# Kernel tuning notes

Measured on AMD Instinct MI355X. Metric: run time of the kernel, lower is better.

The kernel has to match this reference:

```python
import jax, jax.numpy as jnp
import numpy as np

N = 8192        # nodes
F_IN = 128      # input features (layers_dims[0])
F_OUT = 64      # per-head output features (layers_dims[1])
H = 4           # nheads
ALPHA = 0.2     # leaky relu slope
DENSITY = 0.01  # edge density for the random graph


def setup_inputs() -> dict:
    key = jax.random.key(0)
    kx, ka, kw, k1, k2 = jax.random.split(key, 5)
    x = jax.random.normal(kx, (N, F_IN), dtype=jnp.float32)
    adj = (jax.random.uniform(ka, (N, N)) < DENSITY).astype(jnp.float32)
    adj = jnp.maximum(adj, jnp.eye(N, dtype=jnp.float32))
    W = jax.random.normal(kw, (H, F_IN, F_OUT), dtype=jnp.float32) * (1.0 / np.sqrt(F_IN))
    a1 = jax.random.normal(k1, (H, F_OUT), dtype=jnp.float32) * (1.0 / np.sqrt(F_OUT))
    a2 = jax.random.normal(k2, (H, F_OUT), dtype=jnp.float32) * (1.0 / np.sqrt(F_OUT))
    return {"x": x, "adj": adj, "W": W, "a1": a1, "a2": a2}


def reference(x, adj, W, a1, a2):
    # Dropout layers are identity in eval mode (training=False).
    # Per-head projection: Wh[h] = x @ W[h]  -> [H, N, F_OUT]
    Wh = jnp.einsum('nf,hfo->hno', x, W)
    # e_ij = leakyReLU(a1 . Wh_i + a2 . Wh_j) via rank-1 broadcast (classic GAT trick)
    f1 = jnp.einsum('hno,ho->hn', Wh, a1)   # [H, N] (dst contribution)
    f2 = jnp.einsum('hno,ho->hn', Wh, a2)   # [H, N] (src contribution)
    e = f1[:, :, None] + f2[:, None, :]     # [H, N, N]
    e = jnp.where(e > 0, e, ALPHA * e)      # leaky relu
    # mask non-edges, softmax over neighbors (last axis)
    e = jnp.where(adj[None, :, :] > 0, e, jnp.float32(-1e9))
    att = jax.nn.softmax(e, axis=-1)        # [H, N, N]
    # aggregate and apply elu (concat=True branch)
    out = jnp.einsum('hnm,hmo->hno', att, Wh)  # [H, N, F_OUT]
    out = jax.nn.elu(out)
    # concat heads on feature dim -> [N, H*F_OUT]
    return jnp.transpose(out, (1, 0, 2)).reshape(N, H * F_OUT)
```

## Files before the change

### kernel.cpp

```cpp
#include <hip/hip_runtime.h>
#include <math.h>

#define N_NODES 8192
#define F_IN    128
#define F_OUT   64
#define NH      4
#define FC      256
#define MAXDEG  512

__global__ __launch_bounds__(256) void k_proj(const float* __restrict__ x,
                                              const float* __restrict__ W,
                                              float* __restrict__ Wh) {
    __shared__ float xs[16][128];
    __shared__ float ws[32][256];
    const int t = threadIdx.x;
    const int row0 = blockIdx.x * 16;

    {
        const float4* xg = (const float4*)(x + (size_t)row0 * F_IN);
        float4* xls = (float4*)&xs[0][0];
        xls[t]       = xg[t];
        xls[t + 256] = xg[t + 256];
    }

    const int tx = t & 31;
    const int ty = t >> 5;
    const int c0 = tx * 8;
    const int r0 = ty * 2;

    float acc[2][8];
#pragma unroll
    for (int r = 0; r < 2; r++)
#pragma unroll
        for (int c = 0; c < 8; c++) acc[r][c] = 0.f;

    for (int kt = 0; kt < 4; kt++) {
        __syncthreads();
        for (int q = t; q < 2048; q += 256) {
            int krow = q >> 6;
            int c4 = (q & 63) * 4;
            int h = c4 >> 6;
            int o = c4 & 63;
            float4 v = *(const float4*)(W + (size_t)h * (F_IN * F_OUT)
                                          + (size_t)(kt * 32 + krow) * F_OUT + o);
            *(float4*)&ws[krow][c4] = v;
        }
        __syncthreads();
#pragma unroll
        for (int kk4 = 0; kk4 < 8; kk4++) {
            float4 xa0 = *(const float4*)&xs[r0][kt * 32 + kk4 * 4];
            float4 xa1 = *(const float4*)&xs[r0 + 1][kt * 32 + kk4 * 4];
            float a0k[4] = {xa0.x, xa0.y, xa0.z, xa0.w};
            float a1k[4] = {xa1.x, xa1.y, xa1.z, xa1.w};
#pragma unroll
            for (int kkk = 0; kkk < 4; kkk++) {
                int wrow = kk4 * 4 + kkk;
                float4 b0 = *(const float4*)&ws[wrow][c0];
                float4 b1 = *(const float4*)&ws[wrow][c0 + 4];
                float a0 = a0k[kkk], a1v = a1k[kkk];
                acc[0][0] += a0 * b0.x; acc[0][1] += a0 * b0.y;
                acc[0][2] += a0 * b0.z; acc[0][3] += a0 * b0.w;
                acc[0][4] += a0 * b1.x; acc[0][5] += a0 * b1.y;
                acc[0][6] += a0 * b1.z; acc[0][7] += a0 * b1.w;
                acc[1][0] += a1v * b0.x; acc[1][1] += a1v * b0.y;
                acc[1][2] += a1v * b0.z; acc[1][3] += a1v * b0.w;
                acc[1][4] += a1v * b1.x; acc[1][5] += a1v * b1.y;
                acc[1][6] += a1v * b1.z; acc[1][7] += a1v * b1.w;
            }
        }
    }

#pragma unroll
    for (int r = 0; r < 2; r++) {
        float4 v0 = make_float4(acc[r][0], acc[r][1], acc[r][2], acc[r][3]);
        float4 v1 = make_float4(acc[r][4], acc[r][5], acc[r][6], acc[r][7]);
        size_t base = (size_t)(row0 + r0 + r) * FC + c0;
        *(float4*)&Wh[base]     = v0;
        *(float4*)&Wh[base + 4] = v1;
    }
}

__global__ __launch_bounds__(256) void k_f(const float* __restrict__ Wh,
                                           const float* __restrict__ a1,
                                           const float* __restrict__ a2,
                                           float* __restrict__ f1,
                                           float* __restrict__ f2) {
    const int wv = threadIdx.x >> 6;
    const int lane = threadIdx.x & 63;
    const int idx = blockIdx.x * 4 + wv;
    const int n = idx >> 2;
    const int h = idx & 3;
    float w = Wh[(size_t)n * FC + h * F_OUT + lane];
    float s1 = w * a1[h * F_OUT + lane];
    float s2 = w * a2[h * F_OUT + lane];
#pragma unroll
    for (int d = 32; d > 0; d >>= 1) {
        s1 += __shfl_xor(s1, d, 64);
        s2 += __shfl_xor(s2, d, 64);
    }
    if (lane == 0) {
        f1[idx] = s1;
        f2[idx] = s2;
    }
}

__global__ __launch_bounds__(256) void k_gat(const float* __restrict__ adj,
                                             const float* __restrict__ Wh,
                                             const float* __restrict__ f1,
                                             const float* __restrict__ f2,
                                             float* __restrict__ out) {
    __shared__ int cnt;
    __shared__ int jlist[MAXDEG];
    __shared__ float pbuf[NH][MAXDEG];

    const int i = blockIdx.x;
    const int t = threadIdx.x;
    if (t == 0) cnt = 0;
    __syncthreads();

    const float4* arow = (const float4*)(adj + (size_t)i * N_NODES);
    for (int q = t; q < N_NODES / 4; q += 256) {
        float4 v = arow[q];
        int jb = q * 4;
        if (v.x > 0.f) { int p = atomicAdd(&cnt, 1); if (p < MAXDEG) jlist[p] = jb; }
        if (v.y > 0.f) { int p = atomicAdd(&cnt, 1); if (p < MAXDEG) jlist[p] = jb + 1; }
        if (v.z > 0.f) { int p = atomicAdd(&cnt, 1); if (p < MAXDEG) jlist[p] = jb + 2; }
        if (v.w > 0.f) { int p = atomicAdd(&cnt, 1); if (p < MAXDEG) jlist[p] = jb + 3; }
    }
    __syncthreads();
    const int deg = min(cnt, MAXDEG);

    const int h = t >> 6;
    const int lane = t & 63;
    const float f1i = f1[i * 4 + h];

    float m = -1e30f;
    for (int e = lane; e < deg; e += 64) {
        int j = jlist[e];
        float s = f1i + f2[j * 4 + h];
        s = s > 0.f ? s : 0.2f * s;
        pbuf[h][e] = s;
        m = fmaxf(m, s);
    }
#pragma unroll
    for (int d = 32; d > 0; d >>= 1) m = fmaxf(m, __shfl_xor(m, d, 64));

    float l = 0.f;
    for (int e = lane; e < deg; e += 64) {
        float pv = __expf(pbuf[h][e] - m);
        pbuf[h][e] = pv;
        l += pv;
    }
#pragma unroll
    for (int d = 32; d > 0; d >>= 1) l += __shfl_xor(l, d, 64);
    const float inv = 1.f / l;

    __syncthreads();

    float acc0 = 0.f, acc1 = 0.f, acc2 = 0.f, acc3 = 0.f;
    const float* whh = Wh + h * F_OUT + lane;
    int e = 0;
    for (; e + 4 <= deg; e += 4) {
        int j0 = jlist[e], j1 = jlist[e + 1], j2 = jlist[e + 2], j3 = jlist[e + 3];
        float p0 = pbuf[h][e], p1 = pbuf[h][e + 1], p2 = pbuf[h][e + 2], p3 = pbuf[h][e + 3];
        float w0 = whh[(size_t)j0 * FC];
        float w1 = whh[(size_t)j1 * FC];
        float w2 = whh[(size_t)j2 * FC];
        float w3 = whh[(size_t)j3 * FC];
        acc0 += p0 * w0; acc1 += p1 * w1; acc2 += p2 * w2; acc3 += p3 * w3;
    }
    for (; e < deg; e++) {
        acc0 += pbuf[h][e] * whh[(size_t)jlist[e] * FC];
    }
    float v = (acc0 + acc1 + acc2 + acc3) * inv;
    v = v > 0.f ? v : (expf(v) - 1.f);
    out[(size_t)i * FC + t] = v;
}

extern "C" void kernel_launch(void* const* d_in, const int* in_sizes, int n_in,
                              void* d_out, int out_size, void* d_ws, size_t ws_size,
                              hipStream_t stream) {
    const float* x   = (const float*)d_in[0];
    const float* adj = (const float*)d_in[1];
    const float* W   = (const float*)d_in[2];
    const float* a1  = (const float*)d_in[3];
    const float* a2  = (const float*)d_in[4];
    float* out = (float*)d_out;

    float* Wh = (float*)d_ws;
    float* f1 = Wh + (size_t)N_NODES * FC;
    float* f2 = f1 + (size_t)N_NODES * NH;

    k_proj<<<N_NODES / 16, 256, 0, stream>>>(x, W, Wh);
    k_f<<<N_NODES, 256, 0, stream>>>(Wh, a1, a2, f1, f2);
    k_gat<<<N_NODES, 256, 0, stream>>>(adj, Wh, f1, f2, out);
}
```

Baseline: 430.0 us.

## Fuse attention-score projection into GEMM and gather bf16 features in aggregation

Computes f1/f2 inside the projection kernel via a cross-lane reduction, removing the separate k_f launch. Writes a bf16 copy of Wh and gathers it in the attention kernel to halve neighbor-gather bytes. Also uses nontemporal loads for the adjacency stream, drops a redundant barrier, and uses fast exp in ELU. Trades precision of the aggregation for bandwidth and still writes an unused fp32 Wh.

```diff
diff --git a/kernel.cpp b/kernel.cpp
--- a/kernel.cpp
+++ b/kernel.cpp
@@ -1,4 +1,5 @@
 #include <hip/hip_runtime.h>
+#include <hip/hip_bf16.h>
 #include <math.h>
 
 #define N_NODES 8192
@@ -8,9 +9,16 @@
 #define FC      256
 #define MAXDEG  512
 
+typedef float f32x4 __attribute__((ext_vector_type(4)));
+
 __global__ __launch_bounds__(256) void k_proj(const float* __restrict__ x,
                                               const float* __restrict__ W,
-                                              float* __restrict__ Wh) {
+                                              const float* __restrict__ a1,
+                                              const float* __restrict__ a2,
+                                              float* __restrict__ Wh,
+                                              __hip_bfloat16* __restrict__ Wh16,
+                                              float* __restrict__ f1,
+                                              float* __restrict__ f2) {
     __shared__ float xs[16][128];
     __shared__ float ws[32][256];
     const int t = threadIdx.x;
@@ -23,89 +31,87 @@
         xls[t + 256] = xg[t + 256];
     }
 
-    const int tx = t & 31;
-    const int ty = t >> 5;
-    const int c0 = tx * 8;
-    const int r0 = ty * 2;
-
-    float acc[2][8];
-#pragma unroll
-    for (int r = 0; r < 2; r++)
-#pragma unroll
-        for (int c = 0; c < 8; c++) acc[r][c] = 0.f;
+    const int tx = t & 63;
+    const int ty = t >> 6;
+    const int c0 = tx * 4;
+    const int r0 = ty * 4;
+    const int h  = tx >> 4;
+
+    float acc[4][4];
+#pragma unroll
+    for (int r = 0; r < 4; r++)
+#pragma unroll
+        for (int c = 0; c < 4; c++) acc[r][c] = 0.f;
 
     for (int kt = 0; kt < 4; kt++) {
         __syncthreads();
         for (int q = t; q < 2048; q += 256) {
             int krow = q >> 6;
             int c4 = (q & 63) * 4;
-            int h = c4 >> 6;
-            int o = c4 & 63;
-            float4 v = *(const float4*)(W + (size_t)h * (F_IN * F_OUT)
-                                          + (size_t)(kt * 32 + krow) * F_OUT + o);
-            *(float4*)&ws[krow][c4] = v;
+            int hh = c4 >> 6;
+            int o  = c4 & 63;
+            *(float4*)&ws[krow][c4] =
+                *(const float4*)(W + (size_t)hh * (F_IN * F_OUT)
+                                   + (size_t)(kt * 32 + krow) * F_OUT + o);
         }
         __syncthreads();
 #pragma unroll
-        for (int kk4 = 0; kk4 < 8; kk4++) {
-            float4 xa0 = *(const float4*)&xs[r0][kt * 32 + kk4 * 4];
-            float4 xa1 = *(const float4*)&xs[r0 + 1][kt * 32 + kk4 * 4];
+        for (int kg = 0; kg < 8; kg++) {
+            const int kb = kt * 32 + kg * 4;
+            float4 xa0 = *(const float4*)&xs[r0 + 0][kb];
+            float4 xa1 = *(const float4*)&xs[r0 + 1][kb];
+            float4 xa2 = *(const float4*)&xs[r0 + 2][kb];
+            float4 xa3 = *(const float4*)&xs[r0 + 3][kb];
             float a0k[4] = {xa0.x, xa0.y, xa0.z, xa0.w};
             float a1k[4] = {xa1.x, xa1.y, xa1.z, xa1.w};
-#pragma unroll
-            for (int kkk = 0; kkk < 4; kkk++) {
-                int wrow = kk4 * 4 + kkk;
-                float4 b0 = *(const float4*)&ws[wrow][c0];
-                float4 b1 = *(const float4*)&ws[wrow][c0 + 4];
-                float a0 = a0k[kkk], a1v = a1k[kkk];
-                acc[0][0] += a0 * b0.x; acc[0][1] += a0 * b0.y;
-                acc[0][2] += a0 * b0.z; acc[0][3] += a0 * b0.w;
-                acc[0][4] += a0 * b1.x; acc[0][5] += a0 * b1.y;
-                acc[0][6] += a0 * b1.z; acc[0][7] += a0 * b1.w;
-                acc[1][0] += a1v * b0.x; acc[1][1] += a1v * b0.y;
-                acc[1][2] += a1v * b0.z; acc[1][3] += a1v * b0.w;
-                acc[1][4] += a1v * b1.x; acc[1][5] += a1v * b1.y;
-                acc[1][6] += a1v * b1.z; acc[1][7] += a1v * b1.w;
+            float a2k[4] = {xa2.x, xa2.y, xa2.z, xa2.w};
+            float a3k[4] = {xa3.x, xa3.y, xa3.z, xa3.w};
+#pragma unroll
+            for (int kk = 0; kk < 4; kk++) {
+                float4 b = *(const float4*)&ws[kg * 4 + kk][c0];
+                acc[0][0] += a0k[kk] * b.x; acc[0][1] += a0k[kk] * b.y;
+                acc[0][2] += a0k[kk] * b.z; acc[0][3] += a0k[kk] * b.w;
+                acc[1][0] += a1k[kk] * b.x; acc[1][1] += a1k[kk] * b.y;
+                acc[1][2] += a1k[kk] * b.z; acc[1][3] += a1k[kk] * b.w;
+                acc[2][0] += a2k[kk] * b.x; acc[2][1] += a2k[kk] * b.y;
+                acc[2][2] += a2k[kk] * b.z; acc[2][3] += a2k[kk] * b.w;
+                acc[3][0] += a3k[kk] * b.x; acc[3][1] += a3k[kk] * b.y;
+                acc[3][2] += a3k[kk] * b.z; acc[3][3] += a3k[kk] * b.w;
             }
         }
     }
 
-#pragma unroll
-    for (int r = 0; r < 2; r++) {
-        float4 v0 = make_float4(acc[r][0], acc[r][1], acc[r][2], acc[r][3]);
-        float4 v1 = make_float4(acc[r][4], acc[r][5], acc[r][6], acc[r][7]);
-        size_t base = (size_t)(row0 + r0 + r) * FC + c0;
-        *(float4*)&Wh[base]     = v0;
-        *(float4*)&Wh[base + 4] = v1;
+    float a1c[4], a2c[4];
+#pragma unroll
+    for (int c = 0; c < 4; c++) { a1c[c] = a1[c0 + c]; a2c[c] = a2[c0 + c]; }
+
+#pragma unroll
+    for (int r = 0; r < 4; r++) {
+        const int row = row0 + r0 + r;
+        float4 v = make_float4(acc[r][0], acc[r][1], acc[r][2], acc[r][3]);
+        *(float4*)&Wh[(size_t)row * FC + c0] = v;
+        union { __hip_bfloat16 hv[4]; uint2 u; } pk;
+        pk.hv[0] = __float2bfloat16(v.x); pk.hv[1] = __float2bfloat16(v.y);
+        pk.hv[2] = __float2bfloat16(v.z); pk.hv[3] = __float2bfloat16(v.w);
+        *(uint2*)(Wh16 + (size_t)row * FC + c0) = pk.u;
+        float s1 = acc[r][0] * a1c[0] + acc[r][1] * a1c[1]
+                 + acc[r][2] * a1c[2] + acc[r][3] * a1c[3];
+        float s2 = acc[r][0] * a2c[0] + acc[r][1] * a2c[1]
+                 + acc[r][2] * a2c[2] + acc[r][3] * a2c[3];
+#pragma unroll
+        for (int d = 1; d < 16; d <<= 1) {
+            s1 += __shfl_xor(s1, d, 64);
+            s2 += __shfl_xor(s2, d, 64);
+        }
+        if ((tx & 15) == 0) {
+            f1[row * NH + h] = s1;
+            f2[row * NH + h] = s2;
+        }
     }
 }
 
-__global__ __launch_bounds__(256) void k_f(const float* __restrict__ Wh,
-                                           const float* __restrict__ a1,
-                                           const float* __restrict__ a2,
-                                           float* __restrict__ f1,
-                                           float* __restrict__ f2) {
-    const int wv = threadIdx.x >> 6;
-    const int lane = threadIdx.x & 63;
-    const int idx = blockIdx.x * 4 + wv;
-    const int n = idx >> 2;
-    const int h = idx & 3;
-    float w = Wh[(size_t)n * FC + h * F_OUT + lane];
-    float s1 = w * a1[h * F_OUT + lane];
-    float s2 = w * a2[h * F_OUT + lane];
-#pragma unroll
-    for (int d = 32; d > 0; d >>= 1) {
-        s1 += __shfl_xor(s1, d, 64);
-        s2 += __shfl_xor(s2, d, 64);
-    }
-    if (lane == 0) {
-        f1[idx] = s1;
-        f2[idx] = s2;
-    }
-}
-
 __global__ __launch_bounds__(256) void k_gat(const float* __restrict__ adj,
-                                             const float* __restrict__ Wh,
+                                             const __hip_bfloat16* __restrict__ Wh16,
                                              const float* __restrict__ f1,
                                              const float* __restrict__ f2,
                                              float* __restrict__ out) {
@@ -118,9 +124,9 @@
     if (t == 0) cnt = 0;
     __syncthreads();
 
-    const float4* arow = (const float4*)(adj + (size_t)i * N_NODES);
+    const f32x4* arow = (const f32x4*)(adj + (size_t)i * N_NODES);
     for (int q = t; q < N_NODES / 4; q += 256) {
-        float4 v = arow[q];
+        f32x4 v = __builtin_nontemporal_load(&arow[q]);
         int jb = q * 4;
         if (v.x > 0.f) { int p = atomicAdd(&cnt, 1); if (p < MAXDEG) jlist[p] = jb; }
         if (v.y > 0.f) { int p = atomicAdd(&cnt, 1); if (p < MAXDEG) jlist[p] = jb + 1; }
@@ -132,12 +138,12 @@
 
     const int h = t >> 6;
     const int lane = t & 63;
-    const float f1i = f1[i * 4 + h];
+    const float f1i = f1[i * NH + h];
 
     float m = -1e30f;
     for (int e = lane; e < deg; e += 64) {
         int j = jlist[e];
-        float s = f1i + f2[j * 4 + h];
+        float s = f1i + f2[j * NH + h];
         s = s > 0.f ? s : 0.2f * s;
         pbuf[h][e] = s;
         m = fmaxf(m, s);
@@ -155,25 +161,24 @@
     for (int d = 32; d > 0; d >>= 1) l += __shfl_xor(l, d, 64);
     const float inv = 1.f / l;
 
-    __syncthreads();
-
     float acc0 = 0.f, acc1 = 0.f, acc2 = 0.f, acc3 = 0.f;
-    const float* whh = Wh + h * F_OUT + lane;
+    const __hip_bfloat16* whh = Wh16 + h * F_OUT + lane;
     int e = 0;
     for (; e + 4 <= deg; e += 4) {
         int j0 = jlist[e], j1 = jlist[e + 1], j2 = jlist[e + 2], j3 = jlist[e + 3];
-        float p0 = pbuf[h][e], p1 = pbuf[h][e + 1], p2 = pbuf[h][e + 2], p3 = pbuf[h][e + 3];
-        float w0 = whh[(size_t)j0 * FC];
-        float w1 = whh[(size_t)j1 * FC];
-        float w2 = whh[(size_t)j2 * FC];
-        float w3 = whh[(size_t)j3 * FC];
+        float p0 = pbuf[h][e], p1 = pbuf[h][e + 1];
+        float p2 = pbuf[h][e + 2], p3 = pbuf[h][e + 3];
+        float w0 = __bfloat162float(whh[(size_t)j0 * FC]);
+        float w1 = __bfloat162float(whh[(size_t)j1 * FC]);
+        float w2 = __bfloat162float(whh[(size_t)j2 * FC]);
+        float w3 = __bfloat162float(whh[(size_t)j3 * FC]);
         acc0 += p0 * w0; acc1 += p1 * w1; acc2 += p2 * w2; acc3 += p3 * w3;
     }
-    for (; e < deg; e++) {
-        acc0 += pbuf[h][e] * whh[(size_t)jlist[e] * FC];
-    }
+    for (; e < deg; e++)
+        acc0 += pbuf[h][e] * __bfloat162float(whh[(size_t)jlist[e] * FC]);
+
     float v = (acc0 + acc1 + acc2 + acc3) * inv;
-    v = v > 0.f ? v : (expf(v) - 1.f);
+    v = v > 0.f ? v : (__expf(v) - 1.f);
     out[(size_t)i * FC + t] = v;
 }
 
@@ -188,10 +193,10 @@
     float* out = (float*)d_out;
 
     float* Wh = (float*)d_ws;
-    float* f1 = Wh + (size_t)N_NODES * FC;
+    __hip_bfloat16* Wh16 = (__hip_bfloat16*)(Wh + (size_t)N_NODES * FC);
+    float* f1 = (float*)(Wh16 + (size_t)N_NODES * FC);
     float* f2 = f1 + (size_t)N_NODES * NH;
 
-    k_proj<<<N_NODES / 16, 256, 0, stream>>>(x, W, Wh);
-    k_f<<<N_NODES, 256, 0, stream>>>(Wh, a1, a2, f1, f2);
-    k_gat<<<N_NODES, 256, 0, stream>>>(adj, Wh, f1, f2, out);
+    k_proj<<<N_NODES / 16, 256, 0, stream>>>(x, W, a1, a2, Wh, Wh16, f1, f2);
+    k_gat<<<N_NODES, 256, 0, stream>>>(adj, Wh16, f1, f2, out);
 }
```

Result: faster. 412.5 us (-4.1%).
